# Performance work log

Measured on AMD Instinct MI355X. Metric: run time of the kernel, lower is better.

## Reference

```python
import jax, jax.numpy as jnp
import numpy as np

D_MODEL = 1024
NUM_HEADS = 16
HEAD_DIM = D_MODEL // NUM_HEADS

def setup_inputs() -> dict:
    key = jax.random.key(0)
    ks = jax.random.split(key, 9)
    B, L = 2, 2048
    s = 1.0 / np.sqrt(D_MODEL)
    return {
        "x":  jax.random.normal(ks[0], (B, L, D_MODEL), dtype=jnp.float32),
        "Wq": jax.random.uniform(ks[1], (D_MODEL, D_MODEL), jnp.float32, -s, s),
        "bq": jax.random.uniform(ks[2], (D_MODEL,), jnp.float32, -s, s),
        "Wk": jax.random.uniform(ks[3], (D_MODEL, D_MODEL), jnp.float32, -s, s),
        "bk": jax.random.uniform(ks[4], (D_MODEL,), jnp.float32, -s, s),
        "Wv": jax.random.uniform(ks[5], (D_MODEL, D_MODEL), jnp.float32, -s, s),
        "bv": jax.random.uniform(ks[6], (D_MODEL,), jnp.float32, -s, s),
        "Wo": jax.random.uniform(ks[7], (D_MODEL, D_MODEL), jnp.float32, -s, s),
        "bo": jax.random.uniform(ks[8], (D_MODEL,), jnp.float32, -s, s),
    }

def _split_heads(t):
    B, L, _ = t.shape
    return t.reshape(B, L, NUM_HEADS, HEAD_DIM).transpose(0, 2, 1, 3)  # [B,H,L,Dh]

def reference(x, Wq, bq, Wk, bk, Wv, bv, Wo, bo):
    # Linear projections (torch Linear: y = x @ W.T + b)
    Q = _split_heads(x @ Wq.T + bq)
    K = _split_heads(x @ Wk.T + bk)
    V = _split_heads(x @ Wv.T + bv)
    scale = 1.0 / jnp.sqrt(jnp.asarray(HEAD_DIM, dtype=x.dtype))
    scores = jnp.einsum('bhqd,bhkd->bhqk', Q, K) * scale  # [B,H,L,L]
    attn_weights = jax.nn.softmax(scores, axis=-1)
    ctx = jnp.einsum('bhqk,bhkd->bhqd', attn_weights, V)  # [B,H,L,Dh]
    B, H, L, Dh = ctx.shape
    ctx = ctx.transpose(0, 2, 1, 3).reshape(B, L, H * Dh)
    out = ctx @ Wo.T + bo  # dropout p=0.0 -> identity
    return (out, attn_weights)
```

## Files before the change

### kernel.cpp

```cpp
#include <hip/hip_runtime.h>

typedef unsigned short u16;
typedef __bf16 bf16x8 __attribute__((ext_vector_type(8)));
typedef float f32x4 __attribute__((ext_vector_type(4)));

#define WSTR 72
#define TSZ (64 * WSTR)

__device__ __forceinline__ u16 f2bf(float f) {
    union { float f; unsigned int u; } v; v.f = f;
    unsigned int u = v.u;
    u += 0x7fffu + ((u >> 16) & 1u);
    return (u16)(u >> 16);
}

__device__ __forceinline__ u16 cvt_bf(float f) {
    __bf16 h = (__bf16)f;
    union { __bf16 h; u16 u; } v; v.h = h; return v.u;
}

__device__ __forceinline__ void gload16(const u16* g, u16* l) {
    __builtin_amdgcn_global_load_lds((const __attribute__((address_space(1))) unsigned int*)(const void*)g,
                                     (__attribute__((address_space(3))) unsigned int*)(void*)l, 16, 0, 0);
}

#define MFMA16(A, B, C) __builtin_amdgcn_mfma_f32_16x16x32_bf16(A, B, C, 0, 0, 0)

#define LGKM_BARRIER() do { \
    asm volatile("s_waitcnt lgkmcnt(0)\n\ts_barrier" ::: "memory"); \
    __builtin_amdgcn_sched_barrier(0); \
} while (0)

__global__ __launch_bounds__(256) void k_cvtX(const float* __restrict__ src, u16* __restrict__ dst) {
    const size_t i = ((size_t)blockIdx.x * 256 + threadIdx.x) * 8;
    float4 v0 = *(const float4*)(src + i);
    float4 v1 = *(const float4*)(src + i + 4);
    u16 o[8];
    o[0] = f2bf(v0.x); o[1] = f2bf(v0.y); o[2] = f2bf(v0.z); o[3] = f2bf(v0.w);
    o[4] = f2bf(v1.x); o[5] = f2bf(v1.y); o[6] = f2bf(v1.z); o[7] = f2bf(v1.w);
    *(uint4*)(dst + i) = *(const uint4*)o;
}

__global__ __launch_bounds__(256) void k_cvtW(const float* __restrict__ w0, const float* __restrict__ w1,
                                              const float* __restrict__ w2, const float* __restrict__ w3,
                                              u16* __restrict__ dst) {
    const int z = blockIdx.z;
    const float* src = z == 0 ? w0 : z == 1 ? w1 : z == 2 ? w2 : w3;
    const size_t i = ((size_t)blockIdx.x * 256 + threadIdx.x) * 8;
    float4 v0 = *(const float4*)(src + i);
    float4 v1 = *(const float4*)(src + i + 4);
    u16 o[8];
    o[0] = f2bf(v0.x); o[1] = f2bf(v0.y); o[2] = f2bf(v0.z); o[3] = f2bf(v0.w);
    o[4] = f2bf(v1.x); o[5] = f2bf(v1.y); o[6] = f2bf(v1.z); o[7] = f2bf(v1.w);
    *(uint4*)(dst + (size_t)z * 1048576 + i) = *(const uint4*)o;
}

__global__ __launch_bounds__(256) void k_qkv(const u16* __restrict__ Xb, const u16* __restrict__ Wb,
                                             const float* __restrict__ bq, const float* __restrict__ bk,
                                             const float* __restrict__ bv,
                                             u16* __restrict__ Q, u16* __restrict__ Kd, u16* __restrict__ Vtmp) {
    __shared__ __align__(16) u16 lA[128 * 32];
    __shared__ __align__(16) u16 lB[128 * 32];
    const int t = threadIdx.x;
    const int n0 = blockIdx.x * 128;
    const int m0 = blockIdx.y * 128;
    const int lane = t & 63, wave = t >> 6;
    const int wm = (wave >> 1) * 64, wn = (wave & 1) * 64;
    const int quad = lane >> 4, m16 = lane & 15;
    const int r4 = t >> 2, c8 = (t & 3) * 8;
    f32x4 acc[4][4] = {};
    for (int k0 = 0; k0 < 1024; k0 += 32) {
        gload16(Xb + (size_t)(m0 + r4) * 1024 + k0 + c8,       &lA[t * 8]);
        gload16(Xb + (size_t)(m0 + 64 + r4) * 1024 + k0 + c8,  &lA[2048 + t * 8]);
        gload16(Wb + (size_t)(n0 + r4) * 1024 + k0 + c8,       &lB[t * 8]);
        gload16(Wb + (size_t)(n0 + 64 + r4) * 1024 + k0 + c8,  &lB[2048 + t * 8]);
        __syncthreads();
        bf16x8 af[4], bfr[4];
#pragma unroll
        for (int i = 0; i < 4; ++i) {
            af[i]  = *(const bf16x8*)(lA + (wm + i * 16 + m16) * 32 + quad * 8);
            bfr[i] = *(const bf16x8*)(lB + (wn + i * 16 + m16) * 32 + quad * 8);
        }
#pragma unroll
        for (int mi = 0; mi < 4; ++mi)
#pragma unroll
            for (int ni = 0; ni < 4; ++ni)
                acc[mi][ni] = MFMA16(af[mi], bfr[ni], acc[mi][ni]);
        __syncthreads();
    }
#pragma unroll
    for (int ni = 0; ni < 4; ++ni) {
        const int gcol = n0 + wn + ni * 16 + m16;
        const int mat = gcol >> 10;
        const int col = gcol & 1023;
        const int h = col >> 6, d = col & 63;
        const float bias = (mat == 0 ? bq : mat == 1 ? bk : bv)[col];
        u16* dst = mat == 0 ? Q : mat == 1 ? Kd : Vtmp;
#pragma unroll
        for (int mi = 0; mi < 4; ++mi)
#pragma unroll
            for (int e = 0; e < 4; ++e) {
                const int row = m0 + wm + mi * 16 + quad * 4 + e;
                const int b = row >> 11, l = row & 2047;
                dst[(((size_t)(b * 16 + h)) * 2048 + l) * 64 + d] = cvt_bf(acc[mi][ni][e] + bias);
            }
    }
}

__global__ __launch_bounds__(256) void k_vtr(const u16* __restrict__ Vtmp, u16* __restrict__ Vt) {
    __shared__ __align__(16) u16 ld[64 * WSTR];
    const int t = threadIdx.x;
    const int bh = blockIdx.y;
    const int l0 = blockIdx.x * 64;
    const int r = t >> 3, c8 = (t & 7) * 8;
    const u16* src = Vtmp + (size_t)bh * 2048 * 64 + (size_t)l0 * 64;
    *(uint4*)&ld[r * WSTR + c8]        = *(const uint4*)(src + (size_t)r * 64 + c8);
    *(uint4*)&ld[(r + 32) * WSTR + c8] = *(const uint4*)(src + (size_t)(r + 32) * 64 + c8);
    __syncthreads();
    u16* dst = Vt + (size_t)bh * 64 * 2048 + l0;
#pragma unroll
    for (int half = 0; half < 2; ++half) {
        const int d = r + half * 32;
        u16 p[8];
#pragma unroll
        for (int i = 0; i < 8; ++i) p[i] = ld[(c8 + i) * WSTR + d];
        *(uint4*)(dst + (size_t)d * 2048 + c8) = *(const uint4*)p;
    }
}

__global__ __launch_bounds__(256) void k_attn(const u16* __restrict__ Q,
                                              const u16* __restrict__ K,
                                              const u16* __restrict__ Vt,
                                              float* __restrict__ attn,
                                              u16* __restrict__ ctx) {
    __shared__ __align__(16) u16 lK[2 * TSZ];
    __shared__ __align__(16) u16 lV[2 * TSZ];
    __shared__ __align__(16) u16 lW[2 * TSZ];
    __shared__ float sred[2][64];
    const int t = threadIdx.x;
    const int bh = blockIdx.x;
    const int m0 = blockIdx.y * 64;
    const int lane = t & 63, wave = t >> 6;
    const int wq = (wave & 1) * 32;
    const int wk = (wave >> 1) * 32;
    const int wm = (wave >> 1) * 32, wn = (wave & 1) * 32;
    const int quad = lane >> 4, m16 = lane & 15;
    const int sr = t >> 3, sc = (t & 7) * 8;
    const u16* Qh = Q + (size_t)bh * 2048 * 64;
    const u16* Kh = K + (size_t)bh * 2048 * 64;
    const u16* Vh = Vt + (size_t)bh * 64 * 2048;
    float* ah = attn + ((size_t)bh << 22) + (size_t)m0 * 2048;

    const float SC = 0.18033688011112042f;

    bf16x8 qf[2][2];
#pragma unroll
    for (int ni = 0; ni < 2; ++ni)
#pragma unroll
        for (int ks = 0; ks < 2; ++ks)
            qf[ni][ks] = *(const bf16x8*)(Qh + (size_t)(m0 + wq + ni * 16 + m16) * 64 + ks * 32 + quad * 8);

    float slane[2] = {0.f, 0.f};
    {
        *(uint4*)&lK[sr * WSTR + sc]        = *(const uint4*)(Kh + (size_t)sr * 64 + sc);
        *(uint4*)&lK[(sr + 32) * WSTR + sc] = *(const uint4*)(Kh + (size_t)(sr + 32) * 64 + sc);
        int buf = 0;
        for (int kt = 0; kt < 32; ++kt) {
            LGKM_BARRIER();
            uint4 kr0, kr1;
            if (kt < 31) {
                const u16* kp = Kh + (size_t)(kt + 1) * 64 * 64;
                kr0 = *(const uint4*)(kp + (size_t)sr * 64 + sc);
                kr1 = *(const uint4*)(kp + (size_t)(sr + 32) * 64 + sc);
            }
            const u16* lKb = &lK[buf * TSZ];
            bf16x8 k00 = *(const bf16x8*)(lKb + (wk + m16) * WSTR + quad * 8);
            bf16x8 k01 = *(const bf16x8*)(lKb + (wk + m16) * WSTR + 32 + quad * 8);
            bf16x8 k10 = *(const bf16x8*)(lKb + (wk + 16 + m16) * WSTR + quad * 8);
            bf16x8 k11 = *(const bf16x8*)(lKb + (wk + 16 + m16) * WSTR + 32 + quad * 8);
            f32x4 sacc[2][2] = {};
            sacc[0][0] = MFMA16(k00, qf[0][0], sacc[0][0]);
            sacc[0][1] = MFMA16(k00, qf[1][0], sacc[0][1]);
            sacc[1][0] = MFMA16(k10, qf[0][0], sacc[1][0]);
            sacc[1][1] = MFMA16(k10, qf[1][0], sacc[1][1]);
            sacc[0][0] = MFMA16(k01, qf[0][1], sacc[0][0]);
            sacc[0][1] = MFMA16(k01, qf[1][1], sacc[0][1]);
            sacc[1][0] = MFMA16(k11, qf[0][1], sacc[1][0]);
            sacc[1][1] = MFMA16(k11, qf[1][1], sacc[1][1]);
#pragma unroll
            for (int mi = 0; mi < 2; ++mi)
#pragma unroll
                for (int e = 0; e < 4; ++e) {
                    slane[0] += __builtin_amdgcn_exp2f(sacc[mi][0][e] * SC);
                    slane[1] += __builtin_amdgcn_exp2f(sacc[mi][1][e] * SC);
                }
            if (kt < 31) {
                u16* dK = &lK[(buf ^ 1) * TSZ];
                *(uint4*)&dK[sr * WSTR + sc]        = kr0;
                *(uint4*)&dK[(sr + 32) * WSTR + sc] = kr1;
            }
            buf ^= 1;
        }
    }
#pragma unroll
    for (int ni = 0; ni < 2; ++ni) {
        slane[ni] += __shfl_xor(slane[ni], 16);
        slane[ni] += __shfl_xor(slane[ni], 32);
    }
    __syncthreads();
    if (quad == 0) {
        sred[wave >> 1][wq + m16]      = slane[0];
        sred[wave >> 1][wq + 16 + m16] = slane[1];
    }
    __syncthreads();
    float inv[2];
    inv[0] = 1.0f / (sred[0][wq + m16]      + sred[1][wq + m16]);
    inv[1] = 1.0f / (sred[0][wq + 16 + m16] + sred[1][wq + 16 + m16]);

    unsigned aoff[2][2], lwoff[2][2];
#pragma unroll
    for (int mi = 0; mi < 2; ++mi)
#pragma unroll
        for (int ni = 0; ni < 2; ++ni) {
            const int q = wq + ni * 16 + m16;
            const int k = wk + mi * 16 + quad * 4;
            aoff[mi][ni]  = (unsigned)(q * 2048 + k);
            lwoff[mi][ni] = (unsigned)(q * WSTR + k);
        }

    f32x4 cacc[2][2] = {};
    bf16x8 vp00 = {}, vp01 = {}, vp10 = {}, vp11 = {};
    {
        *(uint4*)&lK[sr * WSTR + sc]        = *(const uint4*)(Kh + (size_t)sr * 64 + sc);
        *(uint4*)&lK[(sr + 32) * WSTR + sc] = *(const uint4*)(Kh + (size_t)(sr + 32) * 64 + sc);
        *(uint4*)&lV[sr * WSTR + sc]        = *(const uint4*)(Vh + (size_t)sr * 2048 + sc);
        *(uint4*)&lV[(sr + 32) * WSTR + sc] = *(const uint4*)(Vh + (size_t)(sr + 32) * 2048 + sc);
        int buf = 0;
        for (int kt = 0; kt < 32; ++kt) {
            LGKM_BARRIER();
            uint4 kr0, kr1, vr0, vr1;
            if (kt < 31) {
                const u16* kp  = Kh + (size_t)(kt + 1) * 64 * 64;
                const u16* vp2 = Vh + (size_t)(kt + 1) * 64;
                kr0 = *(const uint4*)(kp + (size_t)sr * 64 + sc);
                kr1 = *(const uint4*)(kp + (size_t)(sr + 32) * 64 + sc);
                vr0 = *(const uint4*)(vp2 + (size_t)sr * 2048 + sc);
                vr1 = *(const uint4*)(vp2 + (size_t)(sr + 32) * 2048 + sc);
            }
            const u16* lKb = &lK[buf * TSZ];
            const u16* lVb = &lV[buf * TSZ];
            bf16x8 vn00 = *(const bf16x8*)(lVb + (wn + m16) * WSTR + quad * 8);
            bf16x8 vn01 = *(const bf16x8*)(lVb + (wn + m16) * WSTR + 32 + quad * 8);
            bf16x8 vn10 = *(const bf16x8*)(lVb + (wn + 16 + m16) * WSTR + quad * 8);
            bf16x8 vn11 = *(const bf16x8*)(lVb + (wn + 16 + m16) * WSTR + 32 + quad * 8);
            bf16x8 k00 = *(const bf16x8*)(lKb + (wk + m16) * WSTR + quad * 8);
            bf16x8 k01 = *(const bf16x8*)(lKb + (wk + m16) * WSTR + 32 + quad * 8);
            bf16x8 k10 = *(const bf16x8*)(lKb + (wk + 16 + m16) * WSTR + quad * 8);
            bf16x8 k11 = *(const bf16x8*)(lKb + (wk + 16 + m16) * WSTR + 32 + quad * 8);
            f32x4 sacc[2][2] = {};
            sacc[0][0] = MFMA16(k00, qf[0][0], sacc[0][0]);
            sacc[0][1] = MFMA16(k00, qf[1][0], sacc[0][1]);
            sacc[1][0] = MFMA16(k10, qf[0][0], sacc[1][0]);
            sacc[1][1] = MFMA16(k10, qf[1][0], sacc[1][1]);
            sacc[0][0] = MFMA16(k01, qf[0][1], sacc[0][0]);
            sacc[0][1] = MFMA16(k01, qf[1][1], sacc[0][1]);
            sacc[1][0] = MFMA16(k11, qf[0][1], sacc[1][0]);
            sacc[1][1] = MFMA16(k11, qf[1][1], sacc[1][1]);
#pragma unroll
            for (int mi = 0; mi < 2; ++mi)
#pragma unroll
                for (int ni = 0; ni < 2; ++ni)
#pragma unroll
                    for (int e = 0; e < 4; ++e)
                        sacc[mi][ni][e] = __builtin_amdgcn_exp2f(sacc[mi][ni][e] * SC) * inv[ni];
            u16* lwb = &lW[(kt & 1) * TSZ];
#pragma unroll
            for (int mi = 0; mi < 2; ++mi)
#pragma unroll
                for (int ni = 0; ni < 2; ++ni) {
                    u16 p[4];
                    p[0] = cvt_bf(sacc[mi][ni][0]); p[1] = cvt_bf(sacc[mi][ni][1]);
                    p[2] = cvt_bf(sacc[mi][ni][2]); p[3] = cvt_bf(sacc[mi][ni][3]);
                    *(uint2*)&lwb[lwoff[mi][ni]] = *(const uint2*)p;
                }
            float* ap = ah + kt * 64;
#pragma unroll
            for (int mi = 0; mi < 2; ++mi)
#pragma unroll
                for (int ni = 0; ni < 2; ++ni)
                    *(f32x4*)(ap + aoff[mi][ni]) = sacc[mi][ni];
            if (kt < 31) {
                u16* dK = &lK[(buf ^ 1) * TSZ];
                u16* dV = &lV[(buf ^ 1) * TSZ];
                *(uint4*)&dK[sr * WSTR + sc]        = kr0;
                *(uint4*)&dK[(sr + 32) * WSTR + sc] = kr1;
                *(uint4*)&dV[sr * WSTR + sc]        = vr0;
                *(uint4*)&dV[(sr + 32) * WSTR + sc] = vr1;
            }
            if (kt > 0) {
                const u16* lwp = &lW[((kt - 1) & 1) * TSZ];
                bf16x8 a00 = *(const bf16x8*)(lwp + (wm + m16) * WSTR + quad * 8);
                bf16x8 a01 = *(const bf16x8*)(lwp + (wm + m16) * WSTR + 32 + quad * 8);
                bf16x8 a10 = *(const bf16x8*)(lwp + (wm + 16 + m16) * WSTR + quad * 8);
                bf16x8 a11 = *(const bf16x8*)(lwp + (wm + 16 + m16) * WSTR + 32 + quad * 8);
                cacc[0][0] = MFMA16(a00, vp00, cacc[0][0]);
                cacc[0][1] = MFMA16(a00, vp10, cacc[0][1]);
                cacc[1][0] = MFMA16(a10, vp00, cacc[1][0]);
                cacc[1][1] = MFMA16(a10, vp10, cacc[1][1]);
                cacc[0][0] = MFMA16(a01, vp01, cacc[0][0]);
                cacc[0][1] = MFMA16(a01, vp11, cacc[0][1]);
                cacc[1][0] = MFMA16(a11, vp01, cacc[1][0]);
                cacc[1][1] = MFMA16(a11, vp11, cacc[1][1]);
            }
            vp00 = vn00; vp01 = vn01; vp10 = vn10; vp11 = vn11;
            buf ^= 1;
        }
        __syncthreads();
        const u16* lwp = &lW[(31 & 1) * TSZ];
        bf16x8 a00 = *(const bf16x8*)(lwp + (wm + m16) * WSTR + quad * 8);
        bf16x8 a01 = *(const bf16x8*)(lwp + (wm + m16) * WSTR + 32 + quad * 8);
        bf16x8 a10 = *(const bf16x8*)(lwp + (wm + 16 + m16) * WSTR + quad * 8);
        bf16x8 a11 = *(const bf16x8*)(lwp + (wm + 16 + m16) * WSTR + 32 + quad * 8);
        cacc[0][0] = MFMA16(a00, vp00, cacc[0][0]);
        cacc[0][1] = MFMA16(a00, vp10, cacc[0][1]);
        cacc[1][0] = MFMA16(a10, vp00, cacc[1][0]);
        cacc[1][1] = MFMA16(a10, vp10, cacc[1][1]);
        cacc[0][0] = MFMA16(a01, vp01, cacc[0][0]);
        cacc[0][1] = MFMA16(a01, vp11, cacc[0][1]);
        cacc[1][0] = MFMA16(a11, vp01, cacc[1][0]);
        cacc[1][1] = MFMA16(a11, vp11, cacc[1][1]);
    }

    const int b = bh >> 4, h = bh & 15;
    u16* cp = ctx + ((size_t)b * 2048) * 1024 + h * 64;
#pragma unroll
    for (int mi = 0; mi < 2; ++mi)
#pragma unroll
        for (int ni = 0; ni < 2; ++ni)
#pragma unroll
            for (int e = 0; e < 4; ++e) {
                const int row = m0 + wm + mi * 16 + quad * 4 + e;
                const int col = wn + ni * 16 + m16;
                cp[(size_t)row * 1024 + col] = cvt_bf(cacc[mi][ni][e]);
            }
}

__global__ __launch_bounds__(256) void k_out(const u16* __restrict__ ctx,
                                             const u16* __restrict__ WoB,
                                             const float* __restrict__ bo,
                                             float* __restrict__ out) {
    __shared__ __align__(16) u16 lA[128 * 32];
    __shared__ __align__(16) u16 lB[128 * 32];
    const int t = threadIdx.x;
    const int n0 = blockIdx.x * 128;
    const int m0 = blockIdx.y * 128;
    const int lane = t & 63, wave = t >> 6;
    const int wm = (wave >> 1) * 64, wn = (wave & 1) * 64;
    const int quad = lane >> 4, m16 = lane & 15;
    const int r4 = t >> 2, c8 = (t & 3) * 8;
    f32x4 acc[4][4] = {};
    for (int k0 = 0; k0 < 1024; k0 += 32) {
        gload16(ctx + (size_t)(m0 + r4) * 1024 + k0 + c8,       &lA[t * 8]);
        gload16(ctx + (size_t)(m0 + 64 + r4) * 1024 + k0 + c8,  &lA[2048 + t * 8]);
        gload16(WoB + (size_t)(n0 + r4) * 1024 + k0 + c8,       &lB[t * 8]);
        gload16(WoB + (size_t)(n0 + 64 + r4) * 1024 + k0 + c8,  &lB[2048 + t * 8]);
        __syncthreads();
        bf16x8 af[4], bfr[4];
#pragma unroll
        for (int i = 0; i < 4; ++i) {
            af[i]  = *(const bf16x8*)(lA + (wm + i * 16 + m16) * 32 + quad * 8);
            bfr[i] = *(const bf16x8*)(lB + (wn + i * 16 + m16) * 32 + quad * 8);
        }
#pragma unroll
        for (int mi = 0; mi < 4; ++mi)
#pragma unroll
            for (int ni = 0; ni < 4; ++ni)
                acc[mi][ni] = MFMA16(af[mi], bfr[ni], acc[mi][ni]);
        __syncthreads();
    }
#pragma unroll
    for (int ni = 0; ni < 4; ++ni) {
        const int col = n0 + wn + ni * 16 + m16;
        const float bv = bo[col];
#pragma unroll
        for (int mi = 0; mi < 4; ++mi)
#pragma unroll
            for (int e = 0; e < 4; ++e) {
                const int row = m0 + wm + mi * 16 + quad * 4 + e;
                out[(size_t)row * 1024 + col] = acc[mi][ni][e] + bv;
            }
    }
}

extern "C" void kernel_launch(void* const* d_in, const int* in_sizes, int n_in,
                              void* d_out, int out_size, void* d_ws, size_t ws_size,
                              hipStream_t stream) {
    const float* x  = (const float*)d_in[0];
    const float* Wq = (const float*)d_in[1];
    const float* bq = (const float*)d_in[2];
    const float* Wk = (const float*)d_in[3];
    const float* bk = (const float*)d_in[4];
    const float* Wv = (const float*)d_in[5];
    const float* bv = (const float*)d_in[6];
    const float* Wo = (const float*)d_in[7];
    const float* bo = (const float*)d_in[8];

    float* out_f = (float*)d_out;
    float* attn  = out_f + (size_t)4096 * 1024;

    u16* Xb = (u16*)d_ws;
    u16* Wb = Xb + (size_t)4194304;
    u16* Qb = Wb + (size_t)4194304;
    u16* Kb = Qb + (size_t)4194304;
    u16* Vt = Kb + (size_t)4194304;
    u16* Vtmp = (u16*)attn;

    dim3 blk(256);
    k_cvtX<<<dim3(2048), blk, 0, stream>>>(x, Xb);
    k_cvtW<<<dim3(512, 1, 4), blk, 0, stream>>>(Wq, Wk, Wv, Wo, Wb);
    k_qkv<<<dim3(24, 32), blk, 0, stream>>>(Xb, Wb, bq, bk, bv, Qb, Kb, Vtmp);
    k_vtr<<<dim3(32, 32), blk, 0, stream>>>(Vtmp, Vt);
    k_attn<<<dim3(32, 32), blk, 0, stream>>>(Qb, Kb, Vt, attn, Xb);
    k_out<<<dim3(8, 32), blk, 0, stream>>>(Xb, Wb + (size_t)3072 * 1024, bo, out_f);
}
```

Before: 693.6 us.

## Fuse V transpose into QKV epilogue via LDS staging and raise MFMA priority

```diff
diff --git a/kernel.cpp b/kernel.cpp
--- a/kernel.cpp
+++ b/kernel.cpp
@@ -58,9 +58,10 @@
 __global__ __launch_bounds__(256) void k_qkv(const u16* __restrict__ Xb, const u16* __restrict__ Wb,
                                              const float* __restrict__ bq, const float* __restrict__ bk,
                                              const float* __restrict__ bv,
-                                             u16* __restrict__ Q, u16* __restrict__ Kd, u16* __restrict__ Vtmp) {
+                                             u16* __restrict__ Q, u16* __restrict__ Kd, u16* __restrict__ Vt) {
     __shared__ __align__(16) u16 lA[128 * 32];
     __shared__ __align__(16) u16 lB[128 * 32];
+    __shared__ __align__(16) u16 lE[128 * 72];
     const int t = threadIdx.x;
     const int n0 = blockIdx.x * 128;
     const int m0 = blockIdx.y * 128;
@@ -88,43 +89,47 @@
                 acc[mi][ni] = MFMA16(af[mi], bfr[ni], acc[mi][ni]);
         __syncthreads();
     }
-#pragma unroll
-    for (int ni = 0; ni < 4; ++ni) {
-        const int gcol = n0 + wn + ni * 16 + m16;
-        const int mat = gcol >> 10;
-        const int col = gcol & 1023;
-        const int h = col >> 6, d = col & 63;
-        const float bias = (mat == 0 ? bq : mat == 1 ? bk : bv)[col];
-        u16* dst = mat == 0 ? Q : mat == 1 ? Kd : Vtmp;
-#pragma unroll
-        for (int mi = 0; mi < 4; ++mi)
-#pragma unroll
-            for (int e = 0; e < 4; ++e) {
-                const int row = m0 + wm + mi * 16 + quad * 4 + e;
-                const int b = row >> 11, l = row & 2047;
-                dst[(((size_t)(b * 16 + h)) * 2048 + l) * 64 + d] = cvt_bf(acc[mi][ni][e] + bias);
-            }
-    }
-}
-
-__global__ __launch_bounds__(256) void k_vtr(const u16* __restrict__ Vtmp, u16* __restrict__ Vt) {
-    __shared__ __align__(16) u16 ld[64 * WSTR];
-    const int t = threadIdx.x;
-    const int bh = blockIdx.y;
-    const int l0 = blockIdx.x * 64;
-    const int r = t >> 3, c8 = (t & 7) * 8;
-    const u16* src = Vtmp + (size_t)bh * 2048 * 64 + (size_t)l0 * 64;
-    *(uint4*)&ld[r * WSTR + c8]        = *(const uint4*)(src + (size_t)r * 64 + c8);
-    *(uint4*)&ld[(r + 32) * WSTR + c8] = *(const uint4*)(src + (size_t)(r + 32) * 64 + c8);
-    __syncthreads();
-    u16* dst = Vt + (size_t)bh * 64 * 2048 + l0;
-#pragma unroll
-    for (int half = 0; half < 2; ++half) {
-        const int d = r + half * 32;
-        u16 p[8];
-#pragma unroll
-        for (int i = 0; i < 8; ++i) p[i] = ld[(c8 + i) * WSTR + d];
-        *(uint4*)(dst + (size_t)d * 2048 + c8) = *(const uint4*)p;
+    const int b = m0 >> 11, l0 = m0 & 2047;
+#pragma unroll
+    for (int hx = 0; hx < 2; ++hx) {
+        __syncthreads();
+        if ((wave & 1) == hx) {
+#pragma unroll
+            for (int ni = 0; ni < 4; ++ni) {
+                const int col = n0 + wn + ni * 16 + m16;
+                const int mat = col >> 10;
+                const float bias = (mat == 0 ? bq : mat == 1 ? bk : bv)[col & 1023];
+#pragma unroll
+                for (int mi = 0; mi < 4; ++mi)
+#pragma unroll
+                    for (int e = 0; e < 4; ++e)
+                        lE[(wm + mi * 16 + quad * 4 + e) * 72 + ni * 16 + m16] = cvt_bf(acc[mi][ni][e] + bias);
+            }
+        }
+        __syncthreads();
+        const int gb = n0 + hx * 64;
+        const int mat = gb >> 10, h = (gb & 1023) >> 6;
+        const int bh = b * 16 + h;
+        if (mat < 2) {
+            u16* dst = (mat == 0 ? Q : Kd) + (((size_t)bh * 2048) + l0) * 64;
+            const int r = t >> 1, off = (t & 1) * 32;
+            const u16* s = lE + r * 72 + off;
+            u16* d2 = dst + (size_t)r * 64 + off;
+            *(uint4*)(d2 + 0)  = *(const uint4*)(s + 0);
+            *(uint4*)(d2 + 8)  = *(const uint4*)(s + 8);
+            *(uint4*)(d2 + 16) = *(const uint4*)(s + 16);
+            *(uint4*)(d2 + 24) = *(const uint4*)(s + 24);
+        } else {
+            const int d = t >> 2, ch = t & 3;
+            u16* dst = Vt + ((size_t)bh * 64 + d) * 2048 + l0 + ch * 32;
+#pragma unroll
+            for (int seg = 0; seg < 4; ++seg) {
+                u16 p[8];
+#pragma unroll
+                for (int j = 0; j < 8; ++j) p[j] = lE[(ch * 32 + seg * 8 + j) * 72 + d];
+                *(uint4*)(dst + seg * 8) = *(const uint4*)p;
+            }
+        }
     }
 }
 
@@ -179,6 +184,7 @@
             bf16x8 k10 = *(const bf16x8*)(lKb + (wk + 16 + m16) * WSTR + quad * 8);
             bf16x8 k11 = *(const bf16x8*)(lKb + (wk + 16 + m16) * WSTR + 32 + quad * 8);
             f32x4 sacc[2][2] = {};
+            __builtin_amdgcn_s_setprio(1);
             sacc[0][0] = MFMA16(k00, qf[0][0], sacc[0][0]);
             sacc[0][1] = MFMA16(k00, qf[1][0], sacc[0][1]);
             sacc[1][0] = MFMA16(k10, qf[0][0], sacc[1][0]);
@@ -187,6 +193,7 @@
             sacc[0][1] = MFMA16(k01, qf[1][1], sacc[0][1]);
             sacc[1][0] = MFMA16(k11, qf[0][1], sacc[1][0]);
             sacc[1][1] = MFMA16(k11, qf[1][1], sacc[1][1]);
+            __builtin_amdgcn_s_setprio(0);
 #pragma unroll
             for (int mi = 0; mi < 2; ++mi)
 #pragma unroll
@@ -258,6 +265,7 @@
             bf16x8 k10 = *(const bf16x8*)(lKb + (wk + 16 + m16) * WSTR + quad * 8);
             bf16x8 k11 = *(const bf16x8*)(lKb + (wk + 16 + m16) * WSTR + 32 + quad * 8);
             f32x4 sacc[2][2] = {};
+            __builtin_amdgcn_s_setprio(1);
             sacc[0][0] = MFMA16(k00, qf[0][0], sacc[0][0]);
             sacc[0][1] = MFMA16(k00, qf[1][0], sacc[0][1]);
             sacc[1][0] = MFMA16(k10, qf[0][0], sacc[1][0]);
@@ -266,6 +274,7 @@
             sacc[0][1] = MFMA16(k01, qf[1][1], sacc[0][1]);
             sacc[1][0] = MFMA16(k11, qf[0][1], sacc[1][0]);
             sacc[1][1] = MFMA16(k11, qf[1][1], sacc[1][1]);
+            __builtin_amdgcn_s_setprio(0);
 #pragma unroll
             for (int mi = 0; mi < 2; ++mi)
 #pragma unroll
@@ -303,6 +312,7 @@
                 bf16x8 a01 = *(const bf16x8*)(lwp + (wm + m16) * WSTR + 32 + quad * 8);
                 bf16x8 a10 = *(const bf16x8*)(lwp + (wm + 16 + m16) * WSTR + quad * 8);
                 bf16x8 a11 = *(const bf16x8*)(lwp + (wm + 16 + m16) * WSTR + 32 + quad * 8);
+                __builtin_amdgcn_s_setprio(1);
                 cacc[0][0] = MFMA16(a00, vp00, cacc[0][0]);
                 cacc[0][1] = MFMA16(a00, vp10, cacc[0][1]);
                 cacc[1][0] = MFMA16(a10, vp00, cacc[1][0]);
@@ -311,6 +321,7 @@
                 cacc[0][1] = MFMA16(a01, vp11, cacc[0][1]);
                 cacc[1][0] = MFMA16(a11, vp01, cacc[1][0]);
                 cacc[1][1] = MFMA16(a11, vp11, cacc[1][1]);
+                __builtin_amdgcn_s_setprio(0);
             }
             vp00 = vn00; vp01 = vn01; vp10 = vn10; vp11 = vn11;
             buf ^= 1;
@@ -413,13 +424,11 @@
     u16* Qb = Wb + (size_t)4194304;
     u16* Kb = Qb + (size_t)4194304;
     u16* Vt = Kb + (size_t)4194304;
-    u16* Vtmp = (u16*)attn;
 
     dim3 blk(256);
     k_cvtX<<<dim3(2048), blk, 0, stream>>>(x, Xb);
     k_cvtW<<<dim3(512, 1, 4), blk, 0, stream>>>(Wq, Wk, Wv, Wo, Wb);
-    k_qkv<<<dim3(24, 32), blk, 0, stream>>>(Xb, Wb, bq, bk, bv, Qb, Kb, Vtmp);
-    k_vtr<<<dim3(32, 32), blk, 0, stream>>>(Vtmp, Vt);
+    k_qkv<<<dim3(24, 32), blk, 0, stream>>>(Xb, Wb, bq, bk, bv, Qb, Kb, Vt);
     k_attn<<<dim3(32, 32), blk, 0, stream>>>(Qb, Kb, Vt, attn, Xb);
     k_out<<<dim3(8, 32), blk, 0, stream>>>(Xb, Wb + (size_t)3072 * 1024, bo, out_f);
 }
```

Result: no change. 702.5 us (+1.3%).
